# Kernel tuning notes

Hardware: AMD Instinct MI355X
Metric: run time of the kernel (lower is better)

The kernel has to match this reference:

```python
import math
import jax, jax.numpy as jnp
import numpy as np

B, S, H, D = 2, 2048, 16, 64

def setup_inputs() -> dict:
    key = jax.random.key(0)
    qkv = jax.random.normal(key, (B, S, 3, H, D), dtype=jnp.float32)
    return {"qkv": qkv}

def reference(qkv) -> jnp.ndarray:
    # qkv: [B, S, 3, H, D]
    q = qkv[:, :, 0]  # [B, S, H, D]
    k = qkv[:, :, 1]
    v = qkv[:, :, 2]
    seqlen = qkv.shape[1]
    softmax_scale = 1.0 / math.sqrt(q.shape[-1])
    # scores: [B, H, T, S]
    scores = jnp.einsum('bthd,bshd->bhts', q, k * softmax_scale)
    # additive causal mask with -10000 above the diagonal (matches torch.triu(..., 1))
    causal_mask = jnp.triu(jnp.full((seqlen, seqlen), -10000.0, dtype=scores.dtype), 1)
    scores = scores + causal_mask
    attention = jax.nn.softmax(scores, axis=-1)
    # dropout_p = 0.0 (eval), so no dropout applied
    output = jnp.einsum('bhts,bshd->bthd', attention, v)  # [B, T, H, D]
    return output
```

## Files before the change

kernel.cpp:

```cpp
#include <hip/hip_runtime.h>

typedef __bf16 bf16x8 __attribute__((ext_vector_type(8)));
typedef float f32x4 __attribute__((ext_vector_type(4)));
typedef unsigned int u32;

constexpr int Bc = 2, Sc = 2048, Hc = 16, Dc = 64;
constexpr int QBLK = 64, KVBLK = 64;
constexpr int NT = Sc / QBLK;
constexpr int ROWSTR = 3 * Hc * Dc;
constexpr float QSCALE = 0.125f * 1.4426950408889634f;


template <int CTRL>
static __device__ __forceinline__ float dppf(float x) {
  int xi = __builtin_bit_cast(int, x);
  return __builtin_bit_cast(float,
      __builtin_amdgcn_update_dpp(xi, xi, CTRL, 0xF, 0xF, false));
}
static __device__ __forceinline__ float redmax16(float x) {
  x = fmaxf(x, dppf<0x121>(x));
  x = fmaxf(x, dppf<0x122>(x));
  x = fmaxf(x, dppf<0x124>(x));
  x = fmaxf(x, dppf<0x128>(x));
  return x;
}
static __device__ __forceinline__ float redsum16(float x) {
  x += dppf<0x121>(x);
  x += dppf<0x122>(x);
  x += dppf<0x124>(x);
  x += dppf<0x128>(x);
  return x;
}

static __device__ __forceinline__ u32 pack2(float a, float b) {
  unsigned short x = __builtin_bit_cast(unsigned short, (__bf16)a);
  unsigned short y = __builtin_bit_cast(unsigned short, (__bf16)b);
  return (u32)x | ((u32)y << 16);
}

__global__ __launch_bounds__(256, 2)
void fattn_kernel(const float* __restrict__ qkv, float* __restrict__ out) {
  const int id = blockIdx.x + blockIdx.y * gridDim.x;
  const int swz = (id & 7) * 64 + (id >> 3);
  const int xlow = swz & 15;
  const int xhigh = NT - 1 - xlow;
  const int bh = swz >> 4;
  const int b = bh >> 4, h = bh & 15;

  const int tid = threadIdx.x;
  const int wave = tid >> 6;
  const int lane = tid & 63;
  const int lg = lane >> 4;
  const int li = lane & 15;

  const float* qp = qkv + (size_t)b * Sc * ROWSTR + h * Dc;
  const float* kp = qp + Hc * Dc;
  const float* vp = qp + 2 * Hc * Dc;

  __shared__ __align__(16) char k_s[KVBLK * Dc * 2];
  __shared__ __align__(16) char v_s[Dc * KVBLK * 2];
  __shared__ __align__(16) char p_s[4][16 * KVBLK * 2];
  char* pw = p_s[wave];

  const int qwL = xlow * QBLK + wave * 16;
  const int qwH = xhigh * QBLK + wave * 16;
  bf16x8 qfL[2], qfH[2];
  {
    const float* qrL = qp + (size_t)(qwL + li) * ROWSTR + 8 * lg;
    const float* qrH = qp + (size_t)(qwH + li) * ROWSTR + 8 * lg;
#pragma unroll
    for (int fi = 0; fi < 2; ++fi) {
      f32x4 a0 = *(const f32x4*)(qrL + 32 * fi);
      f32x4 a1 = *(const f32x4*)(qrL + 32 * fi + 4);
      f32x4 b0 = *(const f32x4*)(qrH + 32 * fi);
      f32x4 b1 = *(const f32x4*)(qrH + 32 * fi + 4);
      bf16x8 qa, qb;
#pragma unroll
      for (int j = 0; j < 4; ++j) {
        qa[j] = (__bf16)(a0[j] * QSCALE); qa[j + 4] = (__bf16)(a1[j] * QSCALE);
        qb[j] = (__bf16)(b0[j] * QSCALE); qb[j + 4] = (__bf16)(b1[j] * QSCALE);
      }
      qfL[fi] = qa; qfH[fi] = qb;
    }
  }

  f32x4 oL[4], oH[4];
  float mLr[4], lLr[4], mHr[4], lHr[4];
#pragma unroll
  for (int n = 0; n < 4; ++n) { oL[n] = f32x4{0, 0, 0, 0}; oH[n] = f32x4{0, 0, 0, 0}; }
#pragma unroll
  for (int r = 0; r < 4; ++r) { mLr[r] = -1e30f; lLr[r] = 0.f; mHr[r] = -1e30f; lHr[r] = 0.f; }

  bf16x8 kf[4][2], vf[4][2];

  auto tile_step = [&](const bf16x8 (&qf)[2], f32x4 (&oacc)[4],
                       float (&mrow)[4], float (&lrow)[4], bool diag, int kv0, int qw) {
    f32x4 sacc[4];
#pragma unroll
    for (int n = 0; n < 4; ++n) sacc[n] = f32x4{0, 0, 0, 0};
    __builtin_amdgcn_s_setprio(1);
#pragma unroll
    for (int n = 0; n < 4; ++n)
#pragma unroll
      for (int fi = 0; fi < 2; ++fi)
        sacc[n] = __builtin_amdgcn_mfma_f32_16x16x32_bf16(qf[fi], kf[n][fi], sacc[n], 0, 0, 0);
    __builtin_amdgcn_s_setprio(0);

    if (diag) {
      const int qrow = qw + 4 * lg;
#pragma unroll
      for (int n = 0; n < 4; ++n)
#pragma unroll
        for (int r = 0; r < 4; ++r)
          if (kv0 + 16 * n + li > qrow + r) sacc[n][r] = -1e30f;
    }

    float pm[4];
#pragma unroll
    for (int r = 0; r < 4; ++r) {
      pm[r] = fmaxf(fmaxf(sacc[0][r], sacc[1][r]), fmaxf(sacc[2][r], sacc[3][r]));
      pm[r] = redmax16(pm[r]);
    }

    bool need = false;
#pragma unroll
    for (int r = 0; r < 4; ++r) need = need || (pm[r] > mrow[r] + 8.0f);
    if (__any(need)) {
#pragma unroll
      for (int r = 0; r < 4; ++r) {
        float mnew = fmaxf(mrow[r], pm[r]);
        float scl = __builtin_exp2f(mrow[r] - mnew);
        mrow[r] = mnew;
        lrow[r] *= scl;
#pragma unroll
        for (int n = 0; n < 4; ++n) oacc[n][r] *= scl;
      }
    }

#pragma unroll
    for (int r = 0; r < 4; ++r) {
      float s = 0.f;
#pragma unroll
      for (int n = 0; n < 4; ++n) {
        float p = __builtin_exp2f(sacc[n][r] - mrow[r]);
        sacc[n][r] = p;
        s += p;
      }
      lrow[r] += redsum16(s);
    }

    {
      const int oddli = li & 1;
      const int kvoff = (li & ~1) * 2;
      const int q0 = 4 * lg + 2 * oddli;
      const int sw0 = (q0 & 7) << 4;
      const int sw1 = ((q0 + 1) & 7) << 4;
#pragma unroll
      for (int n = 0; n < 4; ++n) {
        float t0 = oddli ? sacc[n][0] : sacc[n][2];
        float t1 = oddli ? sacc[n][1] : sacc[n][3];
        float r0 = dppf<0xB1>(t0);
        float r1 = dppf<0xB1>(t1);
        float lo0 = oddli ? r0 : sacc[n][0];
        float hi0 = oddli ? sacc[n][2] : r0;
        float lo1 = oddli ? r1 : sacc[n][1];
        float hi1 = oddli ? sacc[n][3] : r1;
        const int base = n * 32 + kvoff;
        *(u32*)(pw + ((q0 * 128 + base) ^ sw0)) = pack2(lo0, hi0);
        *(u32*)(pw + (((q0 + 1) * 128 + base) ^ sw1)) = pack2(lo1, hi1);
      }
    }

#pragma unroll
    for (int ks = 0; ks < 2; ++ks) {
      const int pbyte = (li * 128 + (32 * ks + 8 * lg) * 2) ^ ((li & 7) << 4);
      bf16x8 pa = *(const bf16x8*)(pw + pbyte);
      __builtin_amdgcn_s_setprio(1);
#pragma unroll
      for (int n = 0; n < 4; ++n)
        oacc[n] = __builtin_amdgcn_mfma_f32_16x16x32_bf16(pa, vf[n][ks], oacc[n], 0, 0, 0);
      __builtin_amdgcn_s_setprio(0);
    }
  };

  for (int t = 0; t <= xhigh; ++t) {
    const int kv0 = t * KVBLK;

#pragma unroll
    for (int it = 0; it < 2; ++it) {
      const int u = tid + it * 256, r = u >> 3, g = u & 7;
      const float* ks = kp + (size_t)(kv0 + r) * ROWSTR + g * 8;
      const float* vs = vp + (size_t)(kv0 + r) * ROWSTR + g * 8;
      f32x4 k0 = *(const f32x4*)ks;
      f32x4 k1 = *(const f32x4*)(ks + 4);
      f32x4 v0 = *(const f32x4*)vs;
      f32x4 v1 = *(const f32x4*)(vs + 4);
      bf16x8 kb;
#pragma unroll
      for (int j = 0; j < 4; ++j) { kb[j] = (__bf16)k0[j]; kb[j + 4] = (__bf16)k1[j]; }
      *(bf16x8*)(k_s + ((r * 128 + g * 16) ^ ((r & 7) << 4))) = kb;

      const int odd = r & 1;
      f32x4 tmp = odd ? v0 : v1;
      f32x4 rcv;
#pragma unroll
      for (int j = 0; j < 4; ++j) rcv[j] = dppf<0x128>(tmp[j]);
      const int kvb2 = (r & ~1) * 2;
#pragma unroll
      for (int s = 0; s < 4; ++s) {
        const int dj = (s + g) & 3;
        const float lo = odd ? rcv[dj] : v0[dj];
        const float hi = odd ? v1[dj] : rcv[dj];
        const int d = 8 * g + 4 * odd + dj;
        *(u32*)(v_s + ((d * 128 + kvb2) ^ ((d & 7) << 4))) = pack2(lo, hi);
      }
    }
    __syncthreads();

#pragma unroll
    for (int n = 0; n < 4; ++n) {
      const int krow = 16 * n + li;
      const int sw = (krow & 7) << 4;
#pragma unroll
      for (int fi = 0; fi < 2; ++fi) {
        kf[n][fi] = *(const bf16x8*)(k_s + ((krow * 128 + fi * 64 + lg * 16) ^ sw));
        vf[n][fi] = *(const bf16x8*)(v_s + ((krow * 128 + fi * 64 + lg * 16) ^ sw));
      }
    }

    tile_step(qfH, oH, mHr, lHr, t == xhigh, kv0, qwH);
    if (t <= xlow)
      tile_step(qfL, oL, mLr, lLr, t == xlow, kv0, qwL);

    __syncthreads();
  }

#pragma unroll
  for (int r = 0; r < 4; ++r) {
    const float invH = 1.0f / lHr[r];
    const float invL = 1.0f / lLr[r];
    float* opH = out + ((size_t)(b * Sc + qwH + 4 * lg + r) * Hc + h) * Dc;
    float* opL = out + ((size_t)(b * Sc + qwL + 4 * lg + r) * Hc + h) * Dc;
#pragma unroll
    for (int n = 0; n < 4; ++n) {
      opH[16 * n + li] = oH[n][r] * invH;
      opL[16 * n + li] = oL[n][r] * invL;
    }
  }
}

extern "C" void kernel_launch(void* const* d_in, const int* in_sizes, int n_in,
                              void* d_out, int out_size, void* d_ws, size_t ws_size,
                              hipStream_t stream) {
  const float* qkv = (const float*)d_in[0];
  float* out = (float*)d_out;
  dim3 grid(NT / 2, Bc * Hc);
  fattn_kernel<<<grid, 256, 0, stream>>>(qkv, out);
}
```

Measured before the change: 91.17 us.

## Split high and low query tiles across separate waves in 512-thread blocks

Each block now runs 8 waves: the first four handle the high (long) query tile and the last four the low tile, where before each of four waves processed both tiles in turn. K/V fragments are read from LDS inside the MFMA loops instead of being preloaded into registers, which lowers register pressure so launch bounds can rise to 512 threads and 4 blocks. The K/V staging loop loses its unroll because each thread now loads one row chunk. Low-tile waves sit idle once their tile is finished but still have to join every barrier, so per-block work stays imbalanced.

```diff
diff --git a/kernel.cpp b/kernel.cpp
--- a/kernel.cpp
+++ b/kernel.cpp
@@ -38,7 +38,7 @@
   return (u32)x | ((u32)y << 16);
 }
 
-__global__ __launch_bounds__(256, 2)
+__global__ __launch_bounds__(512, 4)
 void fattn_kernel(const float* __restrict__ qkv, float* __restrict__ out) {
   const int id = blockIdx.x + blockIdx.y * gridDim.x;
   const int swz = (id & 7) * 64 + (id >> 3);
@@ -52,6 +52,10 @@
   const int lane = tid & 63;
   const int lg = lane >> 4;
   const int li = lane & 15;
+  const bool is_h = wave < 4;
+  const int sub = wave & 3;
+  const int myx = is_h ? xhigh : xlow;
+  const int qw = myx * QBLK + sub * 16;
 
   const float* qp = qkv + (size_t)b * Sc * ROWSTR + h * Dc;
   const float* kp = qp + Hc * Dc;
@@ -59,136 +63,37 @@
 
   __shared__ __align__(16) char k_s[KVBLK * Dc * 2];
   __shared__ __align__(16) char v_s[Dc * KVBLK * 2];
-  __shared__ __align__(16) char p_s[4][16 * KVBLK * 2];
+  __shared__ __align__(16) char p_s[8][16 * KVBLK * 2];
   char* pw = p_s[wave];
 
-  const int qwL = xlow * QBLK + wave * 16;
-  const int qwH = xhigh * QBLK + wave * 16;
-  bf16x8 qfL[2], qfH[2];
+  bf16x8 qf[2];
   {
-    const float* qrL = qp + (size_t)(qwL + li) * ROWSTR + 8 * lg;
-    const float* qrH = qp + (size_t)(qwH + li) * ROWSTR + 8 * lg;
+    const float* qr = qp + (size_t)(qw + li) * ROWSTR + 8 * lg;
 #pragma unroll
     for (int fi = 0; fi < 2; ++fi) {
-      f32x4 a0 = *(const f32x4*)(qrL + 32 * fi);
-      f32x4 a1 = *(const f32x4*)(qrL + 32 * fi + 4);
-      f32x4 b0 = *(const f32x4*)(qrH + 32 * fi);
-      f32x4 b1 = *(const f32x4*)(qrH + 32 * fi + 4);
-      bf16x8 qa, qb;
+      f32x4 a0 = *(const f32x4*)(qr + 32 * fi);
+      f32x4 a1 = *(const f32x4*)(qr + 32 * fi + 4);
+      bf16x8 qa;
 #pragma unroll
       for (int j = 0; j < 4; ++j) {
         qa[j] = (__bf16)(a0[j] * QSCALE); qa[j + 4] = (__bf16)(a1[j] * QSCALE);
-        qb[j] = (__bf16)(b0[j] * QSCALE); qb[j + 4] = (__bf16)(b1[j] * QSCALE);
-      }
-      qfL[fi] = qa; qfH[fi] = qb;
+      }
+      qf[fi] = qa;
     }
   }
 
-  f32x4 oL[4], oH[4];
-  float mLr[4], lLr[4], mHr[4], lHr[4];
-#pragma unroll
-  for (int n = 0; n < 4; ++n) { oL[n] = f32x4{0, 0, 0, 0}; oH[n] = f32x4{0, 0, 0, 0}; }
-#pragma unroll
-  for (int r = 0; r < 4; ++r) { mLr[r] = -1e30f; lLr[r] = 0.f; mHr[r] = -1e30f; lHr[r] = 0.f; }
-
-  bf16x8 kf[4][2], vf[4][2];
-
-  auto tile_step = [&](const bf16x8 (&qf)[2], f32x4 (&oacc)[4],
-                       float (&mrow)[4], float (&lrow)[4], bool diag, int kv0, int qw) {
-    f32x4 sacc[4];
-#pragma unroll
-    for (int n = 0; n < 4; ++n) sacc[n] = f32x4{0, 0, 0, 0};
-    __builtin_amdgcn_s_setprio(1);
-#pragma unroll
-    for (int n = 0; n < 4; ++n)
-#pragma unroll
-      for (int fi = 0; fi < 2; ++fi)
-        sacc[n] = __builtin_amdgcn_mfma_f32_16x16x32_bf16(qf[fi], kf[n][fi], sacc[n], 0, 0, 0);
-    __builtin_amdgcn_s_setprio(0);
-
-    if (diag) {
-      const int qrow = qw + 4 * lg;
-#pragma unroll
-      for (int n = 0; n < 4; ++n)
-#pragma unroll
-        for (int r = 0; r < 4; ++r)
-          if (kv0 + 16 * n + li > qrow + r) sacc[n][r] = -1e30f;
-    }
-
-    float pm[4];
-#pragma unroll
-    for (int r = 0; r < 4; ++r) {
-      pm[r] = fmaxf(fmaxf(sacc[0][r], sacc[1][r]), fmaxf(sacc[2][r], sacc[3][r]));
-      pm[r] = redmax16(pm[r]);
-    }
-
-    bool need = false;
-#pragma unroll
-    for (int r = 0; r < 4; ++r) need = need || (pm[r] > mrow[r] + 8.0f);
-    if (__any(need)) {
-#pragma unroll
-      for (int r = 0; r < 4; ++r) {
-        float mnew = fmaxf(mrow[r], pm[r]);
-        float scl = __builtin_exp2f(mrow[r] - mnew);
-        mrow[r] = mnew;
-        lrow[r] *= scl;
-#pragma unroll
-        for (int n = 0; n < 4; ++n) oacc[n][r] *= scl;
-      }
-    }
-
-#pragma unroll
-    for (int r = 0; r < 4; ++r) {
-      float s = 0.f;
-#pragma unroll
-      for (int n = 0; n < 4; ++n) {
-        float p = __builtin_exp2f(sacc[n][r] - mrow[r]);
-        sacc[n][r] = p;
-        s += p;
-      }
-      lrow[r] += redsum16(s);
-    }
-
-    {
-      const int oddli = li & 1;
-      const int kvoff = (li & ~1) * 2;
-      const int q0 = 4 * lg + 2 * oddli;
-      const int sw0 = (q0 & 7) << 4;
-      const int sw1 = ((q0 + 1) & 7) << 4;
-#pragma unroll
-      for (int n = 0; n < 4; ++n) {
-        float t0 = oddli ? sacc[n][0] : sacc[n][2];
-        float t1 = oddli ? sacc[n][1] : sacc[n][3];
-        float r0 = dppf<0xB1>(t0);
-        float r1 = dppf<0xB1>(t1);
-        float lo0 = oddli ? r0 : sacc[n][0];
-        float hi0 = oddli ? sacc[n][2] : r0;
-        float lo1 = oddli ? r1 : sacc[n][1];
-        float hi1 = oddli ? sacc[n][3] : r1;
-        const int base = n * 32 + kvoff;
-        *(u32*)(pw + ((q0 * 128 + base) ^ sw0)) = pack2(lo0, hi0);
-        *(u32*)(pw + (((q0 + 1) * 128 + base) ^ sw1)) = pack2(lo1, hi1);
-      }
-    }
-
-#pragma unroll
-    for (int ks = 0; ks < 2; ++ks) {
-      const int pbyte = (li * 128 + (32 * ks + 8 * lg) * 2) ^ ((li & 7) << 4);
-      bf16x8 pa = *(const bf16x8*)(pw + pbyte);
-      __builtin_amdgcn_s_setprio(1);
-#pragma unroll
-      for (int n = 0; n < 4; ++n)
-        oacc[n] = __builtin_amdgcn_mfma_f32_16x16x32_bf16(pa, vf[n][ks], oacc[n], 0, 0, 0);
-      __builtin_amdgcn_s_setprio(0);
-    }
-  };
+  f32x4 oacc[4];
+  float mrow[4], lrow[4];
+#pragma unroll
+  for (int n = 0; n < 4; ++n) oacc[n] = f32x4{0, 0, 0, 0};
+#pragma unroll
+  for (int r = 0; r < 4; ++r) { mrow[r] = -1e30f; lrow[r] = 0.f; }
 
   for (int t = 0; t <= xhigh; ++t) {
     const int kv0 = t * KVBLK;
 
-#pragma unroll
-    for (int it = 0; it < 2; ++it) {
-      const int u = tid + it * 256, r = u >> 3, g = u & 7;
+    {
+      const int r = tid >> 3, g = tid & 7;
       const float* ks = kp + (size_t)(kv0 + r) * ROWSTR + g * 8;
       const float* vs = vp + (size_t)(kv0 + r) * ROWSTR + g * 8;
       f32x4 k0 = *(const f32x4*)ks;
@@ -217,35 +122,113 @@
     }
     __syncthreads();
 
-#pragma unroll
-    for (int n = 0; n < 4; ++n) {
-      const int krow = 16 * n + li;
-      const int sw = (krow & 7) << 4;
-#pragma unroll
-      for (int fi = 0; fi < 2; ++fi) {
-        kf[n][fi] = *(const bf16x8*)(k_s + ((krow * 128 + fi * 64 + lg * 16) ^ sw));
-        vf[n][fi] = *(const bf16x8*)(v_s + ((krow * 128 + fi * 64 + lg * 16) ^ sw));
+    if (t <= myx) {
+      f32x4 sacc[4];
+#pragma unroll
+      for (int n = 0; n < 4; ++n) sacc[n] = f32x4{0, 0, 0, 0};
+      __builtin_amdgcn_s_setprio(1);
+#pragma unroll
+      for (int n = 0; n < 4; ++n) {
+        const int krow = 16 * n + li;
+        const int sw = (krow & 7) << 4;
+#pragma unroll
+        for (int fi = 0; fi < 2; ++fi) {
+          bf16x8 kb = *(const bf16x8*)(k_s + ((krow * 128 + fi * 64 + lg * 16) ^ sw));
+          sacc[n] = __builtin_amdgcn_mfma_f32_16x16x32_bf16(qf[fi], kb, sacc[n], 0, 0, 0);
+        }
+      }
+      __builtin_amdgcn_s_setprio(0);
+
+      if (t == myx) {
+        const int qrow = qw + 4 * lg;
+#pragma unroll
+        for (int n = 0; n < 4; ++n)
+#pragma unroll
+          for (int r = 0; r < 4; ++r)
+            if (kv0 + 16 * n + li > qrow + r) sacc[n][r] = -1e30f;
+      }
+
+      float pm[4];
+#pragma unroll
+      for (int r = 0; r < 4; ++r) {
+        pm[r] = fmaxf(fmaxf(sacc[0][r], sacc[1][r]), fmaxf(sacc[2][r], sacc[3][r]));
+        pm[r] = redmax16(pm[r]);
+      }
+
+      bool need = false;
+#pragma unroll
+      for (int r = 0; r < 4; ++r) need = need || (pm[r] > mrow[r] + 8.0f);
+      if (__any(need)) {
+#pragma unroll
+        for (int r = 0; r < 4; ++r) {
+          float mnew = fmaxf(mrow[r], pm[r]);
+          float scl = __builtin_exp2f(mrow[r] - mnew);
+          mrow[r] = mnew;
+          lrow[r] *= scl;
+#pragma unroll
+          for (int n = 0; n < 4; ++n) oacc[n][r] *= scl;
+        }
+      }
+
+#pragma unroll
+      for (int r = 0; r < 4; ++r) {
+        float s = 0.f;
+#pragma unroll
+        for (int n = 0; n < 4; ++n) {
+          float p = __builtin_exp2f(sacc[n][r] - mrow[r]);
+          sacc[n][r] = p;
+          s += p;
+        }
+        lrow[r] += redsum16(s);
+      }
+
+      {
+        const int oddli = li & 1;
+        const int kvoff = (li & ~1) * 2;
+        const int q0 = 4 * lg + 2 * oddli;
+        const int sw0 = (q0 & 7) << 4;
+        const int sw1 = ((q0 + 1) & 7) << 4;
+#pragma unroll
+        for (int n = 0; n < 4; ++n) {
+          float t0 = oddli ? sacc[n][0] : sacc[n][2];
+          float t1 = oddli ? sacc[n][1] : sacc[n][3];
+          float r0 = dppf<0xB1>(t0);
+          float r1 = dppf<0xB1>(t1);
+          float lo0 = oddli ? r0 : sacc[n][0];
+          float hi0 = oddli ? sacc[n][2] : r0;
+          float lo1 = oddli ? r1 : sacc[n][1];
+          float hi1 = oddli ? sacc[n][3] : r1;
+          const int base = n * 32 + kvoff;
+          *(u32*)(pw + ((q0 * 128 + base) ^ sw0)) = pack2(lo0, hi0);
+          *(u32*)(pw + (((q0 + 1) * 128 + base) ^ sw1)) = pack2(lo1, hi1);
+        }
+      }
+
+#pragma unroll
+      for (int ks = 0; ks < 2; ++ks) {
+        const int pbyte = (li * 128 + (32 * ks + 8 * lg) * 2) ^ ((li & 7) << 4);
+        bf16x8 pa = *(const bf16x8*)(pw + pbyte);
+        __builtin_amdgcn_s_setprio(1);
+#pragma unroll
+        for (int n = 0; n < 4; ++n) {
+          const int row = 16 * n + li;
+          const int vbyte = (row * 128 + (32 * ks + 8 * lg) * 2) ^ ((row & 7) << 4);
+          bf16x8 vb = *(const bf16x8*)(v_s + vbyte);
+          oacc[n] = __builtin_amdgcn_mfma_f32_16x16x32_bf16(pa, vb, oacc[n], 0, 0, 0);
+        }
+        __builtin_amdgcn_s_setprio(0);
       }
     }
-
-    tile_step(qfH, oH, mHr, lHr, t == xhigh, kv0, qwH);
-    if (t <= xlow)
-      tile_step(qfL, oL, mLr, lLr, t == xlow, kv0, qwL);
-
     __syncthreads();
   }
 
 #pragma unroll
   for (int r = 0; r < 4; ++r) {
-    const float invH = 1.0f / lHr[r];
-    const float invL = 1.0f / lLr[r];
-    float* opH = out + ((size_t)(b * Sc + qwH + 4 * lg + r) * Hc + h) * Dc;
-    float* opL = out + ((size_t)(b * Sc + qwL + 4 * lg + r) * Hc + h) * Dc;
-#pragma unroll
-    for (int n = 0; n < 4; ++n) {
-      opH[16 * n + li] = oH[n][r] * invH;
-      opL[16 * n + li] = oL[n][r] * invL;
-    }
+    const float inv = 1.0f / lrow[r];
+    float* op = out + ((size_t)(b * Sc + qw + 4 * lg + r) * Hc + h) * Dc;
+#pragma unroll
+    for (int n = 0; n < 4; ++n)
+      op[16 * n + li] = oacc[n][r] * inv;
   }
 }
 
@@ -255,5 +238,5 @@
   const float* qkv = (const float*)d_in[0];
   float* out = (float*)d_out;
   dim3 grid(NT / 2, Bc * Hc);
-  fattn_kernel<<<grid, 256, 0, stream>>>(qkv, out);
-}
+  fattn_kernel<<<grid, 512, 0, stream>>>(qkv, out);
+}
```

New measurement: 94.74 us. +3.9%, slower.

## Double-buffer K/V tiles in LDS with register prefetch of the next tile

Applied to the files above, without the earlier changes.

Issues the global loads for the next K/V tile into registers before computing on the current tile. The converted bf16 data is written into a second LDS buffer afterward, so the loop needs one barrier per iteration instead of two. This is meant to hide global memory latency behind the MFMA and softmax work. It also raises launch bounds to 3 blocks per CU, which squeezes the register budget while the prefetch adds 32 live floats per thread, so spills are possible.

```diff
diff --git a/kernel.cpp b/kernel.cpp
--- a/kernel.cpp
+++ b/kernel.cpp
@@ -38,7 +38,7 @@
   return (u32)x | ((u32)y << 16);
 }
 
-__global__ __launch_bounds__(256, 2)
+__global__ __launch_bounds__(256, 3)
 void fattn_kernel(const float* __restrict__ qkv, float* __restrict__ out) {
   const int id = blockIdx.x + blockIdx.y * gridDim.x;
   const int swz = (id & 7) * 64 + (id >> 3);
@@ -57,8 +57,8 @@
   const float* kp = qp + Hc * Dc;
   const float* vp = qp + 2 * Hc * Dc;
 
-  __shared__ __align__(16) char k_s[KVBLK * Dc * 2];
-  __shared__ __align__(16) char v_s[Dc * KVBLK * 2];
+  __shared__ __align__(16) char k_s[2][KVBLK * Dc * 2];
+  __shared__ __align__(16) char v_s[2][Dc * KVBLK * 2];
   __shared__ __align__(16) char p_s[4][16 * KVBLK * 2];
   char* pw = p_s[wave];
 
@@ -90,6 +90,48 @@
   for (int n = 0; n < 4; ++n) { oL[n] = f32x4{0, 0, 0, 0}; oH[n] = f32x4{0, 0, 0, 0}; }
 #pragma unroll
   for (int r = 0; r < 4; ++r) { mLr[r] = -1e30f; lLr[r] = 0.f; mHr[r] = -1e30f; lHr[r] = 0.f; }
+
+  const int r_a = tid >> 3, g_a = tid & 7;
+  const int r_b = r_a + 32;
+  f32x4 sk0a, sk1a, sv0a, sv1a, sk0b, sk1b, sv0b, sv1b;
+
+  auto load_kv = [&](int kv0) {
+    const float* ksa = kp + (size_t)(kv0 + r_a) * ROWSTR + g_a * 8;
+    const float* vsa = vp + (size_t)(kv0 + r_a) * ROWSTR + g_a * 8;
+    sk0a = *(const f32x4*)ksa; sk1a = *(const f32x4*)(ksa + 4);
+    sv0a = *(const f32x4*)vsa; sv1a = *(const f32x4*)(vsa + 4);
+    const float* ksb = kp + (size_t)(kv0 + r_b) * ROWSTR + g_a * 8;
+    const float* vsb = vp + (size_t)(kv0 + r_b) * ROWSTR + g_a * 8;
+    sk0b = *(const f32x4*)ksb; sk1b = *(const f32x4*)(ksb + 4);
+    sv0b = *(const f32x4*)vsb; sv1b = *(const f32x4*)(vsb + 4);
+  };
+
+  auto write_unit = [&](char* kd, char* vd, int r, int g,
+                        f32x4 k0, f32x4 k1, f32x4 v0, f32x4 v1) {
+    bf16x8 kb;
+#pragma unroll
+    for (int j = 0; j < 4; ++j) { kb[j] = (__bf16)k0[j]; kb[j + 4] = (__bf16)k1[j]; }
+    *(bf16x8*)(kd + ((r * 128 + g * 16) ^ ((r & 7) << 4))) = kb;
+
+    const int odd = r & 1;
+    f32x4 tmp = odd ? v0 : v1;
+    f32x4 rcv;
+#pragma unroll
+    for (int j = 0; j < 4; ++j) rcv[j] = dppf<0x128>(tmp[j]);
+    const int kvb2 = (r & ~1) * 2;
+#pragma unroll
+    for (int s = 0; s < 4; ++s) {
+      const int dj = (s + g) & 3;
+      const float lo = odd ? rcv[dj] : v0[dj];
+      const float hi = odd ? v1[dj] : rcv[dj];
+      const int d = 8 * g + 4 * odd + dj;
+      *(u32*)(vd + ((d * 128 + kvb2) ^ ((d & 7) << 4))) = pack2(lo, hi);
+    }
+  };
+  auto write_kv = [&](char* kd, char* vd) {
+    write_unit(kd, vd, r_a, g_a, sk0a, sk1a, sv0a, sv1a);
+    write_unit(kd, vd, r_b, g_a, sk0b, sk1b, sv0b, sv1b);
+  };
 
   bf16x8 kf[4][2], vf[4][2];
 
@@ -183,39 +225,14 @@
     }
   };
 
+  load_kv(0);
+  write_kv(k_s[0], v_s[0]);
+  __syncthreads();
+
+  int cur = 0;
   for (int t = 0; t <= xhigh; ++t) {
-    const int kv0 = t * KVBLK;
-
-#pragma unroll
-    for (int it = 0; it < 2; ++it) {
-      const int u = tid + it * 256, r = u >> 3, g = u & 7;
-      const float* ks = kp + (size_t)(kv0 + r) * ROWSTR + g * 8;
-      const float* vs = vp + (size_t)(kv0 + r) * ROWSTR + g * 8;
-      f32x4 k0 = *(const f32x4*)ks;
-      f32x4 k1 = *(const f32x4*)(ks + 4);
-      f32x4 v0 = *(const f32x4*)vs;
-      f32x4 v1 = *(const f32x4*)(vs + 4);
-      bf16x8 kb;
-#pragma unroll
-      for (int j = 0; j < 4; ++j) { kb[j] = (__bf16)k0[j]; kb[j + 4] = (__bf16)k1[j]; }
-      *(bf16x8*)(k_s + ((r * 128 + g * 16) ^ ((r & 7) << 4))) = kb;
-
-      const int odd = r & 1;
-      f32x4 tmp = odd ? v0 : v1;
-      f32x4 rcv;
-#pragma unroll
-      for (int j = 0; j < 4; ++j) rcv[j] = dppf<0x128>(tmp[j]);
-      const int kvb2 = (r & ~1) * 2;
-#pragma unroll
-      for (int s = 0; s < 4; ++s) {
-        const int dj = (s + g) & 3;
-        const float lo = odd ? rcv[dj] : v0[dj];
-        const float hi = odd ? v1[dj] : rcv[dj];
-        const int d = 8 * g + 4 * odd + dj;
-        *(u32*)(v_s + ((d * 128 + kvb2) ^ ((d & 7) << 4))) = pack2(lo, hi);
-      }
-    }
-    __syncthreads();
+    const bool more = (t < xhigh);
+    if (more) load_kv((t + 1) * KVBLK);
 
 #pragma unroll
     for (int n = 0; n < 4; ++n) {
@@ -223,16 +240,19 @@
       const int sw = (krow & 7) << 4;
 #pragma unroll
       for (int fi = 0; fi < 2; ++fi) {
-        kf[n][fi] = *(const bf16x8*)(k_s + ((krow * 128 + fi * 64 + lg * 16) ^ sw));
-        vf[n][fi] = *(const bf16x8*)(v_s + ((krow * 128 + fi * 64 + lg * 16) ^ sw));
-      }
-    }
-
+        kf[n][fi] = *(const bf16x8*)(k_s[cur] + ((krow * 128 + fi * 64 + lg * 16) ^ sw));
+        vf[n][fi] = *(const bf16x8*)(v_s[cur] + ((krow * 128 + fi * 64 + lg * 16) ^ sw));
+      }
+    }
+
+    const int kv0 = t * KVBLK;
     tile_step(qfH, oH, mHr, lHr, t == xhigh, kv0, qwH);
     if (t <= xlow)
       tile_step(qfL, oL, mLr, lLr, t == xlow, kv0, qwL);
 
+    if (more) write_kv(k_s[cur ^ 1], v_s[cur ^ 1]);
     __syncthreads();
+    cur ^= 1;
   }
 
 #pragma unroll
```

After: 201.4 us. 121% more time.
